# Kernel tuning notes

Measured on AMD Instinct MI355X. Metric: run time of the kernel, lower is better.

## Reference

```python
import jax, jax.numpy as jnp
import numpy as np

KS = 3          # deform conv kernel size
N = KS * KS     # sampling points per output pixel
PAD = 1         # zero padding


def _conv3x3(x, w, b):
    out = jax.lax.conv_general_dilated(x, w, (1, 1), ((PAD, PAD), (PAD, PAD)),
                                       dimension_numbers=('NCHW', 'OIHW', 'NCHW'))
    return out + b[None, :, None, None]


def _deform_conv(x, w_p, b_p, w_dc):
    # x: [B,C,H,W]; w_p: [2N,C,3,3]; w_dc: [O,C,3,3]
    B, C, H, W = x.shape
    off = jnp.transpose(_conv3x3(x, w_p, b_p), (0, 2, 3, 1))  # [B,H,W,2N]
    k = jnp.arange(KS, dtype=x.dtype) - (KS - 1) // 2
    pny, pnx = jnp.meshgrid(k, k, indexing='ij')              # kernel grid, row-major
    # base grid starts at 1 because of the zero padding of 1 (stride=1)
    py = jnp.arange(1, H + 1, dtype=x.dtype)[:, None, None] + pny.reshape(-1) + off[..., :N]
    px = jnp.arange(1, W + 1, dtype=x.dtype)[None, :, None] + pnx.reshape(-1) + off[..., N:]
    xp = jnp.pad(x, ((0, 0), (0, 0), (PAD, PAD), (PAD, PAD)))
    Hp, Wp = H + 2 * PAD, W + 2 * PAD
    fy = jnp.floor(jax.lax.stop_gradient(py))
    fx = jnp.floor(jax.lax.stop_gradient(px))
    y0 = jnp.clip(fy, 0, Hp - 1).astype(jnp.int32)
    y1 = jnp.clip(fy + 1, 0, Hp - 1).astype(jnp.int32)
    x0 = jnp.clip(fx, 0, Wp - 1).astype(jnp.int32)
    x1 = jnp.clip(fx + 1, 0, Wp - 1).astype(jnp.int32)
    pyc = jnp.clip(py, 0, Hp - 1)
    pxc = jnp.clip(px, 0, Wp - 1)
    y0f, y1f, x0f, x1f = (a.astype(x.dtype) for a in (y0, y1, x0, x1))
    g_lt = (1 + (y0f - pyc)) * (1 + (x0f - pxc))
    g_rb = (1 - (y1f - pyc)) * (1 - (x1f - pxc))
    g_lb = (1 + (y0f - pyc)) * (1 - (x1f - pxc))
    g_rt = (1 - (y1f - pyc)) * (1 + (x0f - pxc))
    # per-batch gather: [C,Hp,Wp] indexed by [H,W,N] -> [C,H,W,N]
    gat = jax.vmap(lambda im, iy, ix: im[:, iy, ix])
    x_off = (g_lt[:, None] * gat(xp, y0, x0) + g_rb[:, None] * gat(xp, y1, x1)
             + g_lb[:, None] * gat(xp, y0, x1) + g_rt[:, None] * gat(xp, y1, x0))  # [B,C,H,W,N]
    O = w_dc.shape[0]
    # equivalent to reshaping x_off to [B,C,H*KS,W*KS] and conv with stride KS
    return jnp.einsum('bchwn,ocn->bohw', x_off, w_dc.reshape(O, C, N))


def setup_inputs() -> dict:
    key = jax.random.key(0)
    ks = jax.random.split(key, 6)
    B, C, H, W = 4, 2, 2048, 128
    rgb = jax.random.normal(ks[0], (B, C, H, W), jnp.float32)
    sar = jax.random.normal(ks[1], (B, C, H, W), jnp.float32)
    w_fm = jax.random.normal(ks[2], (C, C), jnp.float32) * 0.5   # fsm_fm 1x1, no bias
    w_fs = jax.random.normal(ks[3], (C, C), jnp.float32) * 0.5   # fsm_fs 1x1, no bias
    w_p = jax.random.normal(ks[4], (2 * N, 2 * C, KS, KS), jnp.float32) * 0.05  # offset conv
    b_p = jnp.zeros((2 * N,), jnp.float32)
    w_dc = jax.random.normal(ks[5], (C, 2 * C, KS, KS), jnp.float32) * 0.2      # deform kernel
    return {"rgb": rgb, "sar": sar, "w_fm": w_fm, "w_fs": w_fs,
            "w_p": w_p, "b_p": b_p, "w_dc": w_dc}


def reference(rgb, sar, w_fm, w_fs, w_p, b_p, w_dc):
    B, C, H, W = rgb.shape
    P = 128
    # AdaptiveAvgPool2d((128,128)) with H,W divisible by 128 = exact block mean
    avg = rgb.reshape(B, C, P, H // P, P, W // P).mean(axis=(3, 5))   # [B,C,128,128]
    fm = jax.nn.sigmoid(jnp.einsum('oc,bchw->bohw', w_fm, avg))       # [B,C,128,128]
    mat = jnp.einsum('bchk,bckw->bchw', rgb, fm) + rgb                # rgb.matmul(fm) + rgb
    fs = jnp.einsum('oc,bchw->bohw', w_fs, mat)
    x = jnp.concatenate([sar, fs], axis=1)                            # [B,2C,H,W]
    return _deform_conv(x, w_p, b_p, w_dc)
```

## Files before the change

kernel.cpp:

```cpp
#include <hip/hip_runtime.h>
#include <math.h>

typedef __attribute__((ext_vector_type(2))) _Float16 half2v;
typedef __attribute__((ext_vector_type(2))) float f32x2;
typedef __attribute__((ext_vector_type(4), aligned(8))) unsigned int uint4a;

#define BB 4
#define HH 2048
#define WW 128
#define HP (HH + 2)
#define WP (WW + 2)
#define PP 128
#define ROWS 4

#define BORDER_PER_B (2 * WP + 2 * (HP - 2))

__device__ __forceinline__ half2v b2h(unsigned u) { return __builtin_bit_cast(half2v, u); }
__device__ __forceinline__ unsigned pku(float a, float b) {
    return __builtin_bit_cast(unsigned, __builtin_amdgcn_cvt_pkrtz(a, b));
}
__device__ __forceinline__ float dot2(half2v a, unsigned wb, float c) {
    return __builtin_amdgcn_fdot2(a, b2h(wb), c, false);
}
__device__ __forceinline__ float hlo(unsigned u) { return (float)b2h(u).x; }
__device__ __forceinline__ float hhi(unsigned u) { return (float)b2h(u).y; }

__device__ __forceinline__ void swz_map(int bid, int* b, int* h0) {
    int swz = (bid & 7) * 256 + (bid >> 3);
    *b = swz >> 9;
    *h0 = (swz & 511) * 4;
}

__global__ void k_fm(const float* __restrict__ rgb, const float* __restrict__ w_fm,
                     float* __restrict__ fm, uint2* __restrict__ xph) {
    int j = threadIdx.x;
    int bi = blockIdx.x;
    int tid = bi * 128 + j;

    if (tid < BB * BORDER_PER_B) {
        int b = tid / BORDER_PER_B;
        int r = tid - b * BORDER_PER_B;
        int row, col;
        if (r < WP)          { row = 0;      col = r; }
        else if (r < 2 * WP) { row = HP - 1; col = r - WP; }
        else {
            int q = r - 2 * WP;
            row = 1 + (q >> 1);
            col = (q & 1) ? (WP - 1) : 0;
        }
        xph[((size_t)b * HP + row) * WP + col] = make_uint2(0u, 0u);
    }

    int b = bi >> 7, i = bi & 127;
    const float* r0 = rgb + ((size_t)(b * 2 + 0) * HH + (size_t)i * 16) * WW + j;
    const float* r1 = rgb + ((size_t)(b * 2 + 1) * HH + (size_t)i * 16) * WW + j;
    float s0 = 0.f, s1 = 0.f;
#pragma unroll
    for (int a = 0; a < 16; ++a) { s0 += r0[a * WW]; s1 += r1[a * WW]; }
    s0 *= (1.f / 16.f); s1 *= (1.f / 16.f);
    float f0 = w_fm[0] * s0 + w_fm[1] * s1;
    float f1 = w_fm[2] * s0 + w_fm[3] * s1;
    fm[((size_t)(b * 2 + 0) * PP + i) * PP + j] = 1.f / (1.f + expf(-f0));
    fm[((size_t)(b * 2 + 1) * PP + i) * PP + j] = 1.f / (1.f + expf(-f1));
}

__global__ __launch_bounds__(128) void k_mat(
        const float* __restrict__ rgb, const float* __restrict__ sar,
        const float* __restrict__ w_fs, const float* __restrict__ fm,
        uint2* __restrict__ xph) {
    int w = threadIdx.x;
    int b, h0;
    swz_map(blockIdx.x, &b, &h0);

    const float* rg0 = rgb + ((size_t)(b * 2 + 0) * HH + h0) * WW;
    const float* rg1 = rgb + ((size_t)(b * 2 + 1) * HH + h0) * WW;
    const float* fm0 = fm + (size_t)(b * 2 + 0) * PP * PP;
    const float* fm1 = fm + (size_t)(b * 2 + 1) * PP * PP;

    float acc0[ROWS], acc1[ROWS];
#pragma unroll
    for (int r = 0; r < ROWS; ++r) {
        acc0[r] = rg0[r * WW + w];
        acc1[r] = rg1[r * WW + w];
    }

#pragma unroll 4
    for (int k4 = 0; k4 < PP; k4 += 4) {
        float f0[4], f1[4];
#pragma unroll
        for (int t = 0; t < 4; ++t) {
            f0[t] = fm0[(size_t)(k4 + t) * PP + w];
            f1[t] = fm1[(size_t)(k4 + t) * PP + w];
        }
#pragma unroll
        for (int r = 0; r < ROWS; ++r) {
            float4 a0 = *(const float4*)(rg0 + r * WW + k4);
            float4 a1 = *(const float4*)(rg1 + r * WW + k4);
            acc0[r] += a0.x * f0[0] + a0.y * f0[1] + a0.z * f0[2] + a0.w * f0[3];
            acc1[r] += a1.x * f1[0] + a1.y * f1[1] + a1.z * f1[2] + a1.w * f1[3];
        }
    }

    float wa = w_fs[0], wb = w_fs[1], wc = w_fs[2], wd = w_fs[3];
#pragma unroll
    for (int r = 0; r < ROWS; ++r) {
        float m0 = acc0[r], m1 = acc1[r];
        float fs0 = wa * m0 + wb * m1;
        float fs1 = wc * m0 + wd * m1;
        float s0 = sar[((size_t)(b * 2 + 0) * HH + (h0 + r)) * WW + w];
        float s1 = sar[((size_t)(b * 2 + 1) * HH + (h0 + r)) * WW + w];
        uint2 cell = make_uint2(pku(s0, s1), pku(fs0, fs1));
        xph[((size_t)b * HP + (h0 + r + 1)) * WP + (w + 1)] = cell;
    }
}

__global__ __launch_bounds__(256, 2) void k_deform(
        const float* __restrict__ w_p, const float* __restrict__ b_p,
        const float* __restrict__ w_dc, const uint2* __restrict__ xph,
        float* __restrict__ out) {
    int b, h0;
    swz_map(blockIdx.x, &b, &h0);
    int tid = threadIdx.x;
    int w = tid & 127;
    int h = h0 + ((tid >> 7) << 1);

    const uint2* xb = xph + (size_t)b * HP * WP;
    const unsigned* xbu = (const unsigned*)xb;
    float* outb = out + (size_t)(b * 2) * HH * WW;

    uint2 nbc[4][3];
#pragma unroll
    for (int dy = 0; dy < 4; ++dy)
#pragma unroll
        for (int dx = 0; dx < 3; ++dx)
            nbc[dy][dx] = xb[(h + dy) * WP + (w + dx)];

    f32x2 prs[3][3][4];
#pragma unroll
    for (int ky = 0; ky < 3; ++ky)
#pragma unroll
        for (int kx = 0; kx < 3; ++kx) {
            uint2 cA = nbc[ky][kx], cB = nbc[ky + 1][kx];
            prs[ky][kx][0] = (f32x2){hlo(cA.x), hlo(cB.x)};
            prs[ky][kx][1] = (f32x2){hhi(cA.x), hhi(cB.x)};
            prs[ky][kx][2] = (f32x2){hlo(cA.y), hlo(cB.y)};
            prs[ky][kx][3] = (f32x2){hhi(cA.y), hhi(cB.y)};
        }

    f32x2 off2[18];
#pragma unroll
    for (int r = 0; r < 18; ++r) {
        float bias = b_p[r];
        f32x2 s = (f32x2){bias, bias};
#pragma unroll
        for (int ky = 0; ky < 3; ++ky)
#pragma unroll
            for (int kx = 0; kx < 3; ++kx) {
                const float* wr = w_p + r * 36 + ky * 3 + kx;
                s += wr[0] * prs[ky][kx][0] + wr[9] * prs[ky][kx][1]
                   + wr[18] * prs[ky][kx][2] + wr[27] * prs[ky][kx][3];
            }
        off2[r] = s;
    }

    float acc0[2] = {0.f, 0.f};
    float acc1[2] = {0.f, 0.f};

#pragma unroll
    for (int g = 0; g < 3; ++g) {
        unsigned hg[3][2][4];
        bool adj[3][2];
        uint4a q0[3][2], q1[3][2];

#pragma unroll
        for (int j = 0; j < 3; ++j) {
            int n = g * 3 + j;
            int pny = n / 3 - 1;
            int pnx = n % 3 - 1;
            f32x2 py2 = (f32x2){(float)(h + 1 + pny), (float)(h + 2 + pny)} + off2[n];
            f32x2 px2 = (float)(w + 1 + pnx) + off2[9 + n];
            f32x2 fy2 = {floorf(py2.x), floorf(py2.y)};
            f32x2 fx2 = {floorf(px2.x), floorf(px2.y)};
            f32x2 y0f = {fminf(fmaxf(fy2.x, 0.f), (float)(HP - 1)),
                         fminf(fmaxf(fy2.y, 0.f), (float)(HP - 1))};
            f32x2 y1f = {fminf(fmaxf(fy2.x + 1.f, 0.f), (float)(HP - 1)),
                         fminf(fmaxf(fy2.y + 1.f, 0.f), (float)(HP - 1))};
            f32x2 x0f = {fminf(fmaxf(fx2.x, 0.f), (float)(WP - 1)),
                         fminf(fmaxf(fx2.y, 0.f), (float)(WP - 1))};
            f32x2 x1f = {fminf(fmaxf(fx2.x + 1.f, 0.f), (float)(WP - 1)),
                         fminf(fmaxf(fx2.y + 1.f, 0.f), (float)(WP - 1))};
            f32x2 pyc = {fminf(fmaxf(py2.x, 0.f), (float)(HP - 1)),
                         fminf(fmaxf(py2.y, 0.f), (float)(HP - 1))};
            f32x2 pxc = {fminf(fmaxf(px2.x, 0.f), (float)(WP - 1)),
                         fminf(fmaxf(px2.y, 0.f), (float)(WP - 1))};
            f32x2 ay = 1.f + (y0f - pyc);
            f32x2 by = 1.f - (y1f - pyc);
            f32x2 ax = 1.f + (x0f - pxc);
            f32x2 bx = 1.f - (x1f - pxc);
            f32x2 glt = ay * ax, grb = by * bx, glb = ay * bx, grt = by * ax;

#pragma unroll
            for (int p = 0; p < 2; ++p) {
                int y0 = (int)(p ? y0f.y : y0f.x);
                int y1 = (int)(p ? y1f.y : y1f.x);
                int x0 = (int)(p ? x0f.y : x0f.x);
                int x1 = (int)(p ? x1f.y : x1f.x);
                float g_lt = p ? glt.y : glt.x;
                float g_rb = p ? grb.y : grb.x;
                float g_lb = p ? glb.y : glb.x;
                float g_rt = p ? grt.y : grt.x;
                hg[j][p][0] = pku(g_lt, g_lt);
                hg[j][p][1] = pku(g_rb, g_rb);
                hg[j][p][2] = pku(g_lb, g_lb);
                hg[j][p][3] = pku(g_rt, g_rt);
                adj[j][p] = (x1 > x0);
                q0[j][p] = *(const uint4a*)(xbu + 2 * (y0 * WP + x0));
                q1[j][p] = *(const uint4a*)(xbu + 2 * (y1 * WP + x0));
            }
        }

#pragma unroll
        for (int j = 0; j < 3; ++j) {
            int n = g * 3 + j;
            unsigned wd00 = pku(w_dc[0 * 36 + 0 * 9 + n], w_dc[0 * 36 + 1 * 9 + n]);
            unsigned wd01 = pku(w_dc[0 * 36 + 2 * 9 + n], w_dc[0 * 36 + 3 * 9 + n]);
            unsigned wd10 = pku(w_dc[1 * 36 + 0 * 9 + n], w_dc[1 * 36 + 1 * 9 + n]);
            unsigned wd11 = pku(w_dc[1 * 36 + 2 * 9 + n], w_dc[1 * 36 + 3 * 9 + n]);
#pragma unroll
            for (int p = 0; p < 2; ++p) {
                uint4a a = q0[j][p], c = q1[j][p];
                bool ad = adj[j][p];
                unsigned lt01 = a.x, lt23 = a.y;
                unsigned lb01 = ad ? a.z : a.x, lb23 = ad ? a.w : a.y;
                unsigned rt01 = c.x, rt23 = c.y;
                unsigned rb01 = ad ? c.z : c.x, rb23 = ad ? c.w : c.y;

                half2v h01 = b2h(hg[j][p][0]) * b2h(lt01) + b2h(hg[j][p][1]) * b2h(rb01)
                           + b2h(hg[j][p][2]) * b2h(lb01) + b2h(hg[j][p][3]) * b2h(rt01);
                half2v h23 = b2h(hg[j][p][0]) * b2h(lt23) + b2h(hg[j][p][1]) * b2h(rb23)
                           + b2h(hg[j][p][2]) * b2h(lb23) + b2h(hg[j][p][3]) * b2h(rt23);

                acc0[p] = dot2(h01, wd00, acc0[p]);
                acc0[p] = dot2(h23, wd01, acc0[p]);
                acc1[p] = dot2(h01, wd10, acc1[p]);
                acc1[p] = dot2(h23, wd11, acc1[p]);
            }
        }
    }
#pragma unroll
    for (int p = 0; p < 2; ++p) {
        outb[(h + p) * WW + w] = acc0[p];
        outb[HH * WW + (h + p) * WW + w] = acc1[p];
    }
}

extern "C" void kernel_launch(void* const* d_in, const int* in_sizes, int n_in,
                              void* d_out, int out_size, void* d_ws, size_t ws_size,
                              hipStream_t stream) {
    const float* rgb  = (const float*)d_in[0];
    const float* sar  = (const float*)d_in[1];
    const float* w_fm = (const float*)d_in[2];
    const float* w_fs = (const float*)d_in[3];
    const float* w_p  = (const float*)d_in[4];
    const float* b_p  = (const float*)d_in[5];
    const float* w_dc = (const float*)d_in[6];
    float* out = (float*)d_out;

    float* ws = (float*)d_ws;
    float* fm = ws;
    uint2* xph = (uint2*)(ws + 131072);

    k_fm<<<BB * 128, 128, 0, stream>>>(rgb, w_fm, fm, xph);
    k_mat<<<BB * (HH / ROWS), 128, 0, stream>>>(rgb, sar, w_fs, fm, xph);
    k_deform<<<BB * (HH / 4), 256, 0, stream>>>(w_p, b_p, w_dc, xph, out);
}
```

Before: 67.21 us.

## Interleave fm into k-pairs for packed FMA and shrink deform blocks

k_fm now writes the sigmoid gate matrix as float2 pairs of adjacent k rows, with each block averaging 32 rgb rows. k_mat then does the rgb·fm matmul using two-wide f32 vector multiply-adds with a single float2 load per step. This is meant to cut load and FMA instruction counts in the matmul. k_deform moves from 256-thread blocks with launch_bounds(256,2) to 128-thread blocks covering two rows each, with a matching swizzle, which changes occupancy and scheduling. Summation order in the matmul changes slightly.

Result: faster. 58.43 us (-13.1%).

```diff
diff --git a/kernel.cpp b/kernel.cpp
--- a/kernel.cpp
+++ b/kernel.cpp
@@ -25,14 +25,9 @@
 __device__ __forceinline__ float hlo(unsigned u) { return (float)b2h(u).x; }
 __device__ __forceinline__ float hhi(unsigned u) { return (float)b2h(u).y; }
 
-__device__ __forceinline__ void swz_map(int bid, int* b, int* h0) {
-    int swz = (bid & 7) * 256 + (bid >> 3);
-    *b = swz >> 9;
-    *h0 = (swz & 511) * 4;
-}
 
 __global__ void k_fm(const float* __restrict__ rgb, const float* __restrict__ w_fm,
-                     float* __restrict__ fm, uint2* __restrict__ xph) {
+                     float2* __restrict__ fmp, uint2* __restrict__ xph) {
     int j = threadIdx.x;
     int bi = blockIdx.x;
     int tid = bi * 128 + j;
@@ -51,60 +46,68 @@
         xph[((size_t)b * HP + row) * WP + col] = make_uint2(0u, 0u);
     }
 
-    int b = bi >> 7, i = bi & 127;
-    const float* r0 = rgb + ((size_t)(b * 2 + 0) * HH + (size_t)i * 16) * WW + j;
-    const float* r1 = rgb + ((size_t)(b * 2 + 1) * HH + (size_t)i * 16) * WW + j;
-    float s0 = 0.f, s1 = 0.f;
-#pragma unroll
-    for (int a = 0; a < 16; ++a) { s0 += r0[a * WW]; s1 += r1[a * WW]; }
-    s0 *= (1.f / 16.f); s1 *= (1.f / 16.f);
-    float f0 = w_fm[0] * s0 + w_fm[1] * s1;
-    float f1 = w_fm[2] * s0 + w_fm[3] * s1;
-    fm[((size_t)(b * 2 + 0) * PP + i) * PP + j] = 1.f / (1.f + expf(-f0));
-    fm[((size_t)(b * 2 + 1) * PP + i) * PP + j] = 1.f / (1.f + expf(-f1));
+    int b = bi >> 6, t = bi & 63;
+    const float* r0 = rgb + ((size_t)(b * 2 + 0) * HH + (size_t)t * 32) * WW + j;
+    const float* r1 = rgb + ((size_t)(b * 2 + 1) * HH + (size_t)t * 32) * WW + j;
+    float sA0 = 0.f, sA1 = 0.f, sB0 = 0.f, sB1 = 0.f;
+#pragma unroll
+    for (int a = 0; a < 16; ++a) { sA0 += r0[a * WW]; sA1 += r1[a * WW]; }
+#pragma unroll
+    for (int a = 16; a < 32; ++a) { sB0 += r0[a * WW]; sB1 += r1[a * WW]; }
+    sA0 *= (1.f / 16.f); sA1 *= (1.f / 16.f);
+    sB0 *= (1.f / 16.f); sB1 *= (1.f / 16.f);
+    float fA0 = w_fm[0] * sA0 + w_fm[1] * sA1;
+    float fA1 = w_fm[2] * sA0 + w_fm[3] * sA1;
+    float fB0 = w_fm[0] * sB0 + w_fm[1] * sB1;
+    float fB1 = w_fm[2] * sB0 + w_fm[3] * sB1;
+    float gA0 = 1.f / (1.f + expf(-fA0)), gB0 = 1.f / (1.f + expf(-fB0));
+    float gA1 = 1.f / (1.f + expf(-fA1)), gB1 = 1.f / (1.f + expf(-fB1));
+    fmp[((size_t)(b * 2 + 0) * 64 + t) * PP + j] = make_float2(gA0, gB0);
+    fmp[((size_t)(b * 2 + 1) * 64 + t) * PP + j] = make_float2(gA1, gB1);
 }
 
 __global__ __launch_bounds__(128) void k_mat(
         const float* __restrict__ rgb, const float* __restrict__ sar,
-        const float* __restrict__ w_fs, const float* __restrict__ fm,
+        const float* __restrict__ w_fs, const float2* __restrict__ fmp,
         uint2* __restrict__ xph) {
     int w = threadIdx.x;
-    int b, h0;
-    swz_map(blockIdx.x, &b, &h0);
+    int bid = blockIdx.x;
+    int swz = (bid & 7) * 256 + (bid >> 3);
+    int b = swz >> 9;
+    int h0 = (swz & 511) * 4;
 
     const float* rg0 = rgb + ((size_t)(b * 2 + 0) * HH + h0) * WW;
     const float* rg1 = rgb + ((size_t)(b * 2 + 1) * HH + h0) * WW;
-    const float* fm0 = fm + (size_t)(b * 2 + 0) * PP * PP;
-    const float* fm1 = fm + (size_t)(b * 2 + 1) * PP * PP;
-
-    float acc0[ROWS], acc1[ROWS];
+    const float2* fp0 = fmp + (size_t)(b * 2 + 0) * 64 * PP;
+    const float2* fp1 = fmp + (size_t)(b * 2 + 1) * 64 * PP;
+
+    f32x2 av0[ROWS], av1[ROWS];
 #pragma unroll
     for (int r = 0; r < ROWS; ++r) {
-        acc0[r] = rg0[r * WW + w];
-        acc1[r] = rg1[r * WW + w];
+        av0[r] = (f32x2){rg0[r * WW + w], 0.f};
+        av1[r] = (f32x2){rg1[r * WW + w], 0.f};
     }
 
 #pragma unroll 4
-    for (int k4 = 0; k4 < PP; k4 += 4) {
-        float f0[4], f1[4];
-#pragma unroll
-        for (int t = 0; t < 4; ++t) {
-            f0[t] = fm0[(size_t)(k4 + t) * PP + w];
-            f1[t] = fm1[(size_t)(k4 + t) * PP + w];
-        }
+    for (int t = 0; t < 64; ++t) {
+        float2 f0 = fp0[(size_t)t * PP + w];
+        float2 f1 = fp1[(size_t)t * PP + w];
+        f32x2 fv0 = {f0.x, f0.y};
+        f32x2 fv1 = {f1.x, f1.y};
 #pragma unroll
         for (int r = 0; r < ROWS; ++r) {
-            float4 a0 = *(const float4*)(rg0 + r * WW + k4);
-            float4 a1 = *(const float4*)(rg1 + r * WW + k4);
-            acc0[r] += a0.x * f0[0] + a0.y * f0[1] + a0.z * f0[2] + a0.w * f0[3];
-            acc1[r] += a1.x * f1[0] + a1.y * f1[1] + a1.z * f1[2] + a1.w * f1[3];
+            f32x2 a0 = *(const f32x2*)(rg0 + r * WW + 2 * t);
+            f32x2 a1 = *(const f32x2*)(rg1 + r * WW + 2 * t);
+            av0[r] += a0 * fv0;
+            av1[r] += a1 * fv1;
         }
     }
 
     float wa = w_fs[0], wb = w_fs[1], wc = w_fs[2], wd = w_fs[3];
 #pragma unroll
     for (int r = 0; r < ROWS; ++r) {
-        float m0 = acc0[r], m1 = acc1[r];
+        float m0 = av0[r].x + av0[r].y;
+        float m1 = av1[r].x + av1[r].y;
         float fs0 = wa * m0 + wb * m1;
         float fs1 = wc * m0 + wd * m1;
         float s0 = sar[((size_t)(b * 2 + 0) * HH + (h0 + r)) * WW + w];
@@ -114,15 +117,15 @@
     }
 }
 
-__global__ __launch_bounds__(256, 2) void k_deform(
+__global__ __launch_bounds__(128) void k_deform(
         const float* __restrict__ w_p, const float* __restrict__ b_p,
         const float* __restrict__ w_dc, const uint2* __restrict__ xph,
         float* __restrict__ out) {
-    int b, h0;
-    swz_map(blockIdx.x, &b, &h0);
-    int tid = threadIdx.x;
-    int w = tid & 127;
-    int h = h0 + ((tid >> 7) << 1);
+    int bid = blockIdx.x;
+    int swz = (bid & 7) * 512 + (bid >> 3);
+    int b = swz >> 10;
+    int h = (swz & 1023) * 2;
+    int w = threadIdx.x;
 
     const uint2* xb = xph + (size_t)b * HP * WP;
     const unsigned* xbu = (const unsigned*)xb;
@@ -267,10 +270,10 @@
     float* out = (float*)d_out;
 
     float* ws = (float*)d_ws;
-    float* fm = ws;
+    float2* fmp = (float2*)ws;
     uint2* xph = (uint2*)(ws + 131072);
 
-    k_fm<<<BB * 128, 128, 0, stream>>>(rgb, w_fm, fm, xph);
-    k_mat<<<BB * (HH / ROWS), 128, 0, stream>>>(rgb, sar, w_fs, fm, xph);
-    k_deform<<<BB * (HH / 4), 256, 0, stream>>>(w_p, b_p, w_dc, xph, out);
-}
+    k_fm<<<BB * 64, 128, 0, stream>>>(rgb, w_fm, fmp, xph);
+    k_mat<<<BB * (HH / ROWS), 128, 0, stream>>>(rgb, sar, w_fs, fmp, xph);
+    k_deform<<<BB * (HH / 2), 128, 0, stream>>>(w_p, b_p, w_dc, xph, out);
+}
```
